# Optimization experiments

Hardware: AMD Instinct MI355X
Metric: run time of the kernel (lower is better)

## Reference

```python
import jax, jax.numpy as jnp
import numpy as np

EPS = 1e-5

def conv2d(x, w, pad):
    # x: NCHW, w: OIHW
    return jax.lax.conv_general_dilated(
        x, w, window_strides=(1, 1), padding=[(pad, pad), (pad, pad)],
        dimension_numbers=("NCHW", "OIHW", "NCHW"))

def instnorm(x, gamma=None, beta=None):
    # per-(N,C) normalization over H,W (biased variance, like torch InstanceNorm2d)
    mu = jnp.mean(x, axis=(2, 3), keepdims=True)
    var = jnp.mean((x - mu) ** 2, axis=(2, 3), keepdims=True)
    y = (x - mu) * jax.lax.rsqrt(var + EPS)
    if gamma is not None:
        y = y * gamma[None, :, None, None] + beta[None, :, None, None]
    return y

def ode_rhs(y, W, b):
    # conv -> relu -> instance norm (no affine) -> conv_transpose(same weight) -> -1 (stable)
    z = conv2d(y, W, 1) + b[None, :, None, None]
    z = jax.nn.relu(z)
    z = instnorm(z)
    # ConvTranspose2d with weight W (in,out,kh,kw here square C,C) == conv with
    # channel-swapped, spatially flipped kernel, SAME padding.
    Wt = jnp.transpose(jnp.flip(W, axis=(2, 3)), (1, 0, 2, 3))
    z = conv2d(z, Wt, 1)
    return -z

def ode_block(y, Wbank, bbank):
    # RK4 over t_grid = linspace(0,1,5): 4 steps of dt = 0.25.
    # Piecewise-constant weights: floor(t*4) clamped -> stages 1-3 of step i use
    # bank[i]; stage 4 (at t_{i+1}) uses bank[min(i+1, 3)].
    n = Wbank.shape[0]
    dt = 1.0 / n
    for i in range(n):
        j = min(i + 1, n - 1)
        k1 = ode_rhs(y, Wbank[i], bbank[i])
        k2 = ode_rhs(y + 0.5 * dt * k1, Wbank[i], bbank[i])
        k3 = ode_rhs(y + 0.5 * dt * k2, Wbank[i], bbank[i])
        k4 = ode_rhs(y + dt * k3, Wbank[j], bbank[j])
        y = y + (dt / 6.0) * (k1 + 2.0 * k2 + 2.0 * k3 + k4)
    return y

def avgpool2(x):
    N, C, H, W = x.shape
    return x.reshape(N, C, H // 2, 2, W // 2, 2).mean(axis=(3, 5))

def forward(x, stem_w, stem_b, norm1_g, norm1_b, ode1_W, ode1_b,
            conn1_w, conn1_b, norm3_g, norm3_b, ode2_W, ode2_b,
            conn2_w, conn2_b, norm4_g, norm4_b, ode3_W, ode3_b,
            head_w, head_b):
    x = conv2d(x, stem_w, 1) + stem_b[None, :, None, None]
    x = instnorm(x, norm1_g, norm1_b)
    x = jax.nn.relu(x)
    x = ode_block(x, ode1_W, ode1_b)
    x = conv2d(x, conn1_w, 0) + conn1_b[None, :, None, None]
    x = instnorm(x, norm3_g, norm3_b)
    x = jax.nn.relu(x)
    x = avgpool2(x)
    x = ode_block(x, ode2_W, ode2_b)
    x = conv2d(x, conn2_w, 0) + conn2_b[None, :, None, None]
    x = instnorm(x, norm4_g, norm4_b)
    x = jax.nn.relu(x)
    x = avgpool2(x)
    x = ode_block(x, ode3_W, ode3_b)
    x = x.mean(axis=(2, 3))  # AdaptiveAvgPool2d(1) + Flatten -> [N, 4*ch]
    return x @ head_w.T + head_b

def setup_inputs() -> dict:
    key = jax.random.key(0)
    ks = jax.random.split(key, 16)
    ch = 64
    f = jnp.float32
    d = {
        "x": jax.random.normal(ks[0], (8, 3, 96, 96), f),
        "stem_w": jax.random.normal(ks[1], (ch, 3, 3, 3), f) * 0.1,
        "stem_b": jnp.zeros((ch,), f),
        "norm1_g": jnp.ones((ch,), f),
        "norm1_b": jnp.zeros((ch,), f),
        "ode1_W": jax.random.normal(ks[2], (4, ch, ch, 3, 3), f) * 0.1,
        "ode1_b": jnp.zeros((4, ch), f),
        "conn1_w": jax.random.normal(ks[3], (2 * ch, ch, 1, 1), f) * 0.1,
        "conn1_b": jnp.zeros((2 * ch,), f),
        "norm3_g": jnp.ones((2 * ch,), f),
        "norm3_b": jnp.zeros((2 * ch,), f),
        "ode2_W": jax.random.normal(ks[4], (4, 2 * ch, 2 * ch, 3, 3), f) * 0.1,
        "ode2_b": jnp.zeros((4, 2 * ch), f),
        "conn2_w": jax.random.normal(ks[5], (4 * ch, 2 * ch, 1, 1), f) * 0.1,
        "conn2_b": jnp.zeros((4 * ch,), f),
        "norm4_g": jnp.ones((4 * ch,), f),
        "norm4_b": jnp.zeros((4 * ch,), f),
        "ode3_W": jax.random.normal(ks[6], (4, 4 * ch, 4 * ch, 3, 3), f) * 0.1,
        "ode3_b": jnp.zeros((4, 4 * ch), f),
        "head_w": jax.random.normal(ks[7], (10, 4 * ch), f) * 0.05,
        "head_b": jnp.zeros((10,), f),
    }
    return d

def reference(x, stem_w, stem_b, norm1_g, norm1_b, ode1_W, ode1_b,
              conn1_w, conn1_b, norm3_g, norm3_b, ode2_W, ode2_b,
              conn2_w, conn2_b, norm4_g, norm4_b, ode3_W, ode3_b,
              head_w, head_b):
    return forward(x, stem_w, stem_b, norm1_g, norm1_b, ode1_W, ode1_b,
                   conn1_w, conn1_b, norm3_g, norm3_b, ode2_W, ode2_b,
                   conn2_w, conn2_b, norm4_g, norm4_b, ode3_W, ode3_b,
                   head_w, head_b)
```

## Files before the change

### kernel.cpp

```cpp
#include <hip/hip_runtime.h>


typedef __attribute__((ext_vector_type(8)))  short  s16x8;
typedef __attribute__((ext_vector_type(16))) float  f32x16;

__device__ __forceinline__ unsigned short bf16_rtne(float f) {
    unsigned u = __builtin_bit_cast(unsigned, f);
    unsigned r = u + 0x7FFFu + ((u >> 16) & 1u);
    return (unsigned short)(r >> 16);
}
__device__ __forceinline__ void split2(float v, unsigned& h, unsigned& l) {
    unsigned u = __builtin_bit_cast(unsigned, v);
    h = (u + 0x7fffu + ((u >> 16) & 1u)) >> 16;
    float r = v - __builtin_bit_cast(float, h << 16);
    unsigned ur = __builtin_bit_cast(unsigned, r);
    l = (ur + 0x7fffu + ((ur >> 16) & 1u)) >> 16;
}
__device__ __forceinline__ unsigned packsplit(float v) {
    unsigned h, l; split2(v, h, l); return h | (l << 16);
}

__global__ __launch_bounds__(256) void pack_weights(
    const float* __restrict__ Wb, unsigned short* __restrict__ out, int C)
{
    const int dir = blockIdx.y;
    const int MT = C >> 5, ICC = C >> 4;
    const size_t TOT = (size_t)36 * C * C;
    size_t t = (size_t)blockIdx.x * 256 + threadIdx.x;
    if (t >= TOT) return;
    int j = t & 7;
    int l = (t >> 3) & 63;
    size_t r = t >> 9;
    int kp  = r % 9;  r /= 9;
    int mt  = r % MT; r /= MT;
    int icc = r % ICC; r /= ICC;
    int bank = (int)r;
    int oc = mt * 32 + (l & 31);
    int ic = icc * 16 + (l >> 5) * 8 + j;
    int kh = kp / 3, kw = kp % 3;
    float v;
    if (dir == 0)
        v = Wb[(((size_t)(bank * C + oc) * C + ic) * 3 + kh) * 3 + kw];
    else
        v = Wb[(((size_t)(bank * C + ic) * C + oc) * 3 + (2 - kh)) * 3 + (2 - kw)];
    unsigned short h = bf16_rtne(v);
    float hf = __builtin_bit_cast(float, (unsigned)h << 16);
    unsigned short lo = bf16_rtne(v - hf);
    size_t idx = ((((size_t)bank * ICC + icc) * MT + mt) * 9 + kp) * 1024 + l * 8 + j;
    unsigned short* base = out + (size_t)dir * 72 * C * C;
    base[idx] = h;
    base[idx + 512] = lo;
}

template<int NW, int MODE>
__global__ __launch_bounds__(NW * 64) void conv_mfma4(
    const void* __restrict__ in,
    const unsigned short* __restrict__ pA,
    const float* __restrict__ bias,
    const float* __restrict__ partI,
    float* __restrict__ partO,
    const float* __restrict__ ybase, float* __restrict__ accb,
    float* __restrict__ ydstF, unsigned* __restrict__ ydstS,
    int C, int H, int W, int tilesX, int tilesT, float inv_hw,
    int mode, float acoef, float dt6)
{
    constexpr bool CONV2 = (MODE == 2);
    constexpr int TPX = 16, TPY = 2 * NW;
    constexpr int HX = TPX + 2, HY = TPY + 2;
    constexpr int NROW = HX * HY;
    constexpr int RS = 20;
    constexpr int PL = NROW * RS;
    constexpr int BUFS = 2 * PL;
    constexpr int NTHR = NW * 64;
    constexpr int NELEM = NROW * 16;
    constexpr int NIT = (NELEM + NTHR - 1) / NTHR;
    __shared__ __align__(16) unsigned short sB[2 * BUFS];
    __shared__ float sTab[CONV2 ? 512 : 4];

    const int tid = threadIdx.x;
    const int w = tid >> 6, lane = tid & 63;
    const int n = blockIdx.x;
    const int tile = blockIdx.y;
    const int mt = blockIdx.z;
    const int tileX = tile % tilesX, tileY = tile / tilesX;
    const int px0 = tileX * TPX, py0 = tileY * TPY;
    const int ocb = mt * 32;
    const int HW = H * W;
    const int ICC = C >> 4, MT = C >> 5;
    const int col = lane & 31, half = lane >> 5;
    const int xl = col & 15, yr = col >> 4;
    const int wy0 = 2 * w;
    const int ncbase = n * C;

    float stg[NIT];
    auto stageLoad = [&](int icc) {
#pragma unroll
        for (int i = 0; i < NIT; i++) {
            int e = tid + i * NTHR;
            float v = 0.f;
            if (e < NELEM) {
                int ic = e / NROW; int r = e - ic * NROW;
                int yy = r / HX, xx = r - yy * HX;
                int gy = py0 + yy - 1, gx = px0 + xx - 1;
                if (gy >= 0 && gy < H && gx >= 0 && gx < W) {
                    int c = icc * 16 + ic;
                    size_t ad = (size_t)(ncbase + c) * HW + gy * W + gx;
                    if (MODE == 0)
                        v = ((const float*)in)[ad];
                    else
                        v = __builtin_bit_cast(float, ((const unsigned*)in)[ad]);
                }
            }
            stg[i] = v;
        }
    };
    auto stageWrite = [&](int b, int c0) {
#pragma unroll
        for (int i = 0; i < NIT; i++) {
            int e = tid + i * NTHR;
            if (e < NELEM) {
                int ic = e / NROW; int r = e - ic * NROW;
                unsigned h, l;
                if (MODE == 1) {
                    unsigned u = __builtin_bit_cast(unsigned, stg[i]);
                    h = u & 0xffffu; l = u >> 16;
                } else if (MODE == 2) {
                    int yy = r / HX, xx = r - yy * HX;
                    int gy = py0 + yy - 1, gx = px0 + xx - 1;
                    float v = 0.f;
                    if (gy >= 0 && gy < H && gx >= 0 && gx < W) {
                        unsigned u = __builtin_bit_cast(unsigned, stg[i]);
                        float vh = __builtin_bit_cast(float, u << 16);
                        float vl = __builtin_bit_cast(float, u & 0xffff0000u);
                        int c = c0 + ic;
                        v = (vh + vl - sTab[2 * c]) * sTab[2 * c + 1];
                    }
                    split2(v, h, l);
                } else {
                    split2(stg[i], h, l);
                }
                int off = b * BUFS + r * RS + ic;
                sB[off] = (unsigned short)h;
                sB[off + PL] = (unsigned short)l;
            }
        }
    };
    auto loadB = [&](int b, int kp, s16x8& oh, s16x8& ol) {
        int kh = kp / 3, kw = kp - kh * 3;
        int px = (wy0 + yr + kh) * HX + (xl + kw);
        int off = b * BUFS + px * RS + half * 8;
        oh = *(const s16x8*)&sB[off];
        ol = *(const s16x8*)&sB[off + PL];
    };

    f32x16 accA{}, accB{}, accC{};

    stageLoad(0);

    if (CONV2) {
        float* sRed = (float*)sB;
        const int g = NTHR / C;
        {
            int c0 = tid % C, sl = tid / C;
            int mtc = c0 >> 5, occ = c0 & 31;
            int t0 = (tilesT * sl) / g, t1 = (tilesT * (sl + 1)) / g;
            const float* pb = partI + ((size_t)(n * MT + mtc) * tilesT) * 64 + occ;
            float S = 0.f, Q = 0.f;
            for (int tt = t0; tt < t1; ++tt) {
                S += pb[(size_t)tt * 64];
                Q += pb[(size_t)tt * 64 + 32];
            }
            sRed[tid] = S;
            sRed[NTHR + tid] = Q;
        }
        __syncthreads();
        if (tid < C) {
            float s = 0.f, q = 0.f;
            for (int k = 0; k < g; ++k) {
                s += sRed[k * C + tid];
                q += sRed[NTHR + k * C + tid];
            }
            float m = s * inv_hw;
            sTab[2 * tid] = m;
            sTab[2 * tid + 1] = rsqrtf(fmaf(-m, m, q * inv_hw) + 1e-5f);
        }
        __syncthreads();
    }

    stageWrite(0, 0);
    __syncthreads();

    for (int icc = 0; icc < ICC; ++icc) {
        s16x8 aH[9], aL[9];
        {
            const unsigned short* ab =
                pA + ((size_t)(icc * MT + mt)) * 9216 + lane * 8;
#pragma unroll
            for (int kp = 0; kp < 9; ++kp) {
                aH[kp] = *(const s16x8*)(ab + kp * 1024);
                aL[kp] = *(const s16x8*)(ab + kp * 1024 + 512);
            }
        }
        const int b = icc & 1;
        if (icc + 1 < ICC) stageLoad(icc + 1);

        s16x8 bh, bl;
        loadB(b, 0, bh, bl);
#pragma unroll
        for (int kp = 0; kp < 9; ++kp) {
            s16x8 bhn, bln;
            if (kp < 8) loadB(b, kp + 1, bhn, bln);
            accA = __builtin_amdgcn_mfma_f32_32x32x16_bf16(aH[kp], bh, accA, 0, 0, 0);
            accB = __builtin_amdgcn_mfma_f32_32x32x16_bf16(aL[kp], bh, accB, 0, 0, 0);
            accC = __builtin_amdgcn_mfma_f32_32x32x16_bf16(aH[kp], bl, accC, 0, 0, 0);
            if (kp < 8) { bh = bhn; bl = bln; }
        }
        if (icc + 1 < ICC) {
            stageWrite(b ^ 1, (icc + 1) * 16);
            __syncthreads();
        }
    }

    const int gx = px0 + xl;
    const int gy = py0 + wy0 + yr;
    const bool valid = (gx < W);
    float* sred = (float*)sB;
#pragma unroll
    for (int r = 0; r < 16; r++) {
        int row = (r & 3) + 8 * (r >> 2) + 4 * half;
        int oc = ocb + row;
        size_t idx = (size_t)(ncbase + oc) * HW + (size_t)gy * W + gx;
        float v = accA[r] + accB[r] + accC[r];
        if (!CONV2) {
            v += bias[oc];
            v = fmaxf(v, 0.f);
            if (valid) ydstS[idx] = packsplit(v);
            float s = valid ? v : 0.f;
            float sq = s * s;
#pragma unroll
            for (int m = 1; m < 32; m <<= 1) {
                s  += __shfl_xor(s, m, 64);
                sq += __shfl_xor(sq, m, 64);
            }
            if ((lane & 31) == 0) {
                int slot = ((w * 2 + half) * 16 + r) * 2;
                sred[slot] = s;
                sred[slot + 1] = sq;
            }
        } else if (valid) {
            float k = -v;
            if (mode == 0) {
                accb[idx] = k;
                ydstS[idx] = packsplit(ybase[idx] + acoef * k);
            } else if (mode == 3) {
                ydstF[idx] = ybase[idx] + dt6 * (accb[idx] + k);
            } else {
                accb[idx] += 2.f * k;
                ydstS[idx] = packsplit(ybase[idx] + acoef * k);
            }
        }
    }
    if (!CONV2) {
        __syncthreads();
        if (tid < 32) {
            int h2 = (tid >> 2) & 1;
            int r  = (tid & 3) | ((tid >> 3) << 2);
            float s = 0.f, sq = 0.f;
#pragma unroll
            for (int wv = 0; wv < NW; wv++) {
                int slot = ((wv * 2 + h2) * 16 + r) * 2;
                s  += sred[slot];
                sq += sred[slot + 1];
            }
            float* po = partO + ((size_t)(n * MT + mt) * tilesT + tile) * 64;
            po[tid] = s;
            po[tid + 32] = sq;
        }
    }
}

__global__ __launch_bounds__(256) void conv3x3_stem(
    const float* __restrict__ in, const float* __restrict__ w,
    const float* __restrict__ bias, float* __restrict__ out,
    int H, int W, int tilesX)
{
    __shared__ float sIn[3][18][34];
    __shared__ float sW[16][3][9];
    const int tid = threadIdx.x;
    const int tx = tid & 15, ty = tid >> 4;
    const int tileX = blockIdx.x % tilesX, tileY = blockIdx.x / tilesX;
    const int x0 = tileX * 32, y0 = tileY * 16;
    const int oc0 = blockIdx.y * 16;
    const int n = blockIdx.z;
    const int HW = H * W;

    for (int idx = tid; idx < 3 * 18 * 34; idx += 256) {
        int c = idx / (18 * 34); int r = idx % (18 * 34);
        int iy = r / 34, ix = r % 34;
        int gy = y0 + iy - 1, gx = x0 + ix - 1;
        float v = 0.f;
        if (gy >= 0 && gy < H && gx >= 0 && gx < W)
            v = in[(size_t)(n * 3 + c) * HW + gy * W + gx];
        sIn[c][iy][ix] = v;
    }
    for (int idx = tid; idx < 16 * 27; idx += 256) {
        int o = idx / 27, r = idx % 27;
        sW[o][r / 9][r % 9] = w[(size_t)(oc0 + o) * 27 + r];
    }
    __syncthreads();

    float a0[16], a1[16];
#pragma unroll
    for (int o = 0; o < 16; o++) { a0[o] = 0.f; a1[o] = 0.f; }
#pragma unroll
    for (int c = 0; c < 3; c++)
#pragma unroll
        for (int kh = 0; kh < 3; kh++)
#pragma unroll
            for (int kw = 0; kw < 3; kw++) {
                float v0 = sIn[c][ty + kh][tx + kw];
                float v1 = sIn[c][ty + kh][tx + 16 + kw];
#pragma unroll
                for (int o = 0; o < 16; o++) {
                    float wv = sW[o][c][kh * 3 + kw];
                    a0[o] = fmaf(v0, wv, a0[o]);
                    a1[o] = fmaf(v1, wv, a1[o]);
                }
            }

    const int gy = y0 + ty, gx = x0 + tx;
#pragma unroll
    for (int o = 0; o < 16; o++) {
        float bb = bias[oc0 + o];
        size_t base = (size_t)(n * 64 + oc0 + o) * HW + (size_t)gy * W + gx;
        out[base] = a0[o] + bb;
        out[base + 16] = a1[o] + bb;
    }
}

__global__ __launch_bounds__(256) void stats_kernel(
    const float* __restrict__ x, float* __restrict__ mu, float* __restrict__ rstd,
    int HW, float inv_hw)
{
    int nc = blockIdx.x;
    const float* p = x + (size_t)nc * HW;
    float s = 0.f, ss = 0.f;
    for (int i = threadIdx.x; i < HW; i += 256) {
        float v = p[i];
        s += v;
        ss = fmaf(v, v, ss);
    }
    for (int off = 32; off; off >>= 1) {
        s  += __shfl_down(s, off, 64);
        ss += __shfl_down(ss, off, 64);
    }
    __shared__ float aS[4], aSS[4];
    int wid = threadIdx.x >> 6, lane = threadIdx.x & 63;
    if (lane == 0) { aS[wid] = s; aSS[wid] = ss; }
    __syncthreads();
    if (threadIdx.x == 0) {
        s  = aS[0] + aS[1] + aS[2] + aS[3];
        ss = aSS[0] + aSS[1] + aSS[2] + aSS[3];
        float m = s * inv_hw;
        float var = fmaf(-m, m, ss * inv_hw);
        mu[nc] = m;
        rstd[nc] = rsqrtf(var + 1e-5f);
    }
}

__global__ __launch_bounds__(256) void norm_affine_relu_kernel(
    const float* __restrict__ in, float* __restrict__ out,
    const float* __restrict__ mu, const float* __restrict__ rstd,
    const float* __restrict__ g, const float* __restrict__ b,
    int C, int HW, size_t total)
{
    size_t i = (size_t)blockIdx.x * 256 + threadIdx.x;
    if (i >= total) return;
    size_t nc = i / HW;
    int c = (int)(nc % C);
    float v = (in[i] - mu[nc]) * rstd[nc] * g[c] + b[c];
    out[i] = fmaxf(v, 0.f);
}

__global__ __launch_bounds__(256) void norm_pool_kernel(
    const float* __restrict__ in, float* __restrict__ out,
    const float* __restrict__ mu, const float* __restrict__ rstd,
    const float* __restrict__ g, const float* __restrict__ b,
    int C, int Ho, int Wo, size_t total)
{
    size_t i = (size_t)blockIdx.x * 256 + threadIdx.x;
    if (i >= total) return;
    int wo = (int)(i % Wo);
    int ho = (int)((i / Wo) % Ho);
    size_t nc = i / ((size_t)Wo * Ho);
    int c = (int)(nc % C);
    const int Wi = 2 * Wo;
    const float* p = in + nc * (size_t)(4 * Ho * Wo) + (size_t)(2 * ho) * Wi + 2 * wo;
    float sc  = rstd[nc] * g[c];
    float off = fmaf(-mu[nc], sc, b[c]);
    float2 t0 = *(const float2*)p;
    float2 t1 = *(const float2*)(p + Wi);
    float s = fmaxf(fmaf(t0.x, sc, off), 0.f) + fmaxf(fmaf(t0.y, sc, off), 0.f)
            + fmaxf(fmaf(t1.x, sc, off), 0.f) + fmaxf(fmaf(t1.y, sc, off), 0.f);
    out[i] = 0.25f * s;
}

#define C1OCT 8
__global__ __launch_bounds__(256) void conv1x1_kernel(
    const float* __restrict__ in, const float* __restrict__ w,
    const float* __restrict__ bias, float* __restrict__ out,
    int Cin, int Cout, int HW)
{
    const int HW4 = HW >> 2;
    int p = blockIdx.x * 256 + threadIdx.x;
    if (p >= HW4) return;
    const int oc0 = blockIdx.y * C1OCT;
    const int n = blockIdx.z;
    const float4* ip = (const float4*)(in + (size_t)n * Cin * HW) + p;
    float acc[C1OCT][4];
#pragma unroll
    for (int o = 0; o < C1OCT; o++)
        acc[o][0] = acc[o][1] = acc[o][2] = acc[o][3] = 0.f;
#pragma unroll 4
    for (int ic = 0; ic < Cin; ic++) {
        float4 v = ip[(size_t)ic * HW4];
#pragma unroll
        for (int o = 0; o < C1OCT; o++) {
            float wv = w[(size_t)(oc0 + o) * Cin + ic];
            acc[o][0] = fmaf(v.x, wv, acc[o][0]);
            acc[o][1] = fmaf(v.y, wv, acc[o][1]);
            acc[o][2] = fmaf(v.z, wv, acc[o][2]);
            acc[o][3] = fmaf(v.w, wv, acc[o][3]);
        }
    }
    float4* op = (float4*)(out + ((size_t)n * Cout + oc0) * HW) + p;
#pragma unroll
    for (int o = 0; o < C1OCT; o++) {
        float bb = bias[oc0 + o];
        float4 r;
        r.x = acc[o][0] + bb; r.y = acc[o][1] + bb;
        r.z = acc[o][2] + bb; r.w = acc[o][3] + bb;
        op[(size_t)o * HW4] = r;
    }
}

__global__ __launch_bounds__(128) void head_kernel(
    const float* __restrict__ m, const float* __restrict__ hw,
    const float* __restrict__ hb, float* __restrict__ out, int C)
{
    int t = threadIdx.x;
    if (t < 80) {
        int n = t / 10, k = t % 10;
        float acc = hb[k];
        for (int c = 0; c < C; c++)
            acc = fmaf(m[n * C + c], hw[k * C + c], acc);
        out[t] = acc;
    }
}

struct OdeCfg { int C, H, tilesX, tilesT; };
static const OdeCfg CFG[3] = {
    {64, 96, 6, 72},
    {128, 48, 3, 18},
    {256, 24, 2, 6},
};

static void launch_c1(int st, int inMode, const void* in, const unsigned short* pA,
                      const float* bias, float* part, unsigned* z, hipStream_t s)
{
    const OdeCfg& c = CFG[st];
    dim3 g(8, c.tilesT, c.C / 32);
    float ih = 1.f / (c.H * c.H);
    if (inMode == 0)
        conv_mfma4<4, 0><<<g, 256, 0, s>>>(in, pA, bias,
            nullptr, part, nullptr, nullptr, nullptr, z,
            c.C, c.H, c.H, c.tilesX, c.tilesT, ih, 0, 0.f, 0.f);
    else
        conv_mfma4<4, 1><<<g, 256, 0, s>>>(in, pA, bias,
            nullptr, part, nullptr, nullptr, nullptr, z,
            c.C, c.H, c.H, c.tilesX, c.tilesT, ih, 0, 0.f, 0.f);
}

static void launch_c2(int st, const unsigned* z, const unsigned short* pA,
                      const float* part,
                      const float* ybase, float* accb,
                      float* ydstF, unsigned* ydstS,
                      int mode, float acoef, hipStream_t s)
{
    const OdeCfg& c = CFG[st];
    dim3 g(8, c.tilesT, c.C / 32);
    float ih = 1.f / (c.H * c.H);
    const float dt6 = 0.25f / 6.f;
    conv_mfma4<4, 2><<<g, 256, 0, s>>>(z, pA, nullptr,
        part, nullptr, ybase, accb, ydstF, ydstS,
        c.C, c.H, c.H, c.tilesX, c.tilesT, ih, mode, acoef, dt6);
}

static void ode_block_mfma(int st, float* y, unsigned* t, unsigned* z, float* a,
                           float* part, unsigned short* pack,
                           const float* bbank, hipStream_t s)
{
    const OdeCfg& c = CFG[st];
    const int C = c.C;
    const size_t BANKW = (size_t)18 * C * C;
    const size_t DIRW  = (size_t)72 * C * C;
    const float dt = 0.25f;
    for (int i = 0; i < 4; i++) {
        int j = (i + 1 > 3) ? 3 : i + 1;
        const unsigned short* p1  = pack + i * BANKW;
        const unsigned short* p1t = pack + DIRW + i * BANKW;
        const unsigned short* p4  = pack + j * BANKW;
        const unsigned short* p4t = pack + DIRW + j * BANKW;
        const float* b1 = bbank + (size_t)i * C;
        const float* b4 = bbank + (size_t)j * C;

        launch_c1(st, 0, y, p1, b1, part, z, s);
        launch_c2(st, z, p1t, part, y, a, nullptr, t, 0, 0.5f * dt, s);
        launch_c1(st, 1, t, p1, b1, part, z, s);
        launch_c2(st, z, p1t, part, y, a, nullptr, t, 1, 0.5f * dt, s);
        launch_c1(st, 1, t, p1, b1, part, z, s);
        launch_c2(st, z, p1t, part, y, a, nullptr, t, 1, dt, s);
        launch_c1(st, 1, t, p4, b4, part, z, s);
        launch_c2(st, z, p4t, part, y, a, y, t, 3, 0.f, s);
    }
}

extern "C" void kernel_launch(void* const* d_in, const int* in_sizes, int n_in,
                              void* d_out, int out_size, void* d_ws, size_t ws_size,
                              hipStream_t stream)
{
    const float* x       = (const float*)d_in[0];
    const float* stem_w  = (const float*)d_in[1];
    const float* stem_b  = (const float*)d_in[2];
    const float* norm1_g = (const float*)d_in[3];
    const float* norm1_b = (const float*)d_in[4];
    const float* ode1_W  = (const float*)d_in[5];
    const float* ode1_b  = (const float*)d_in[6];
    const float* conn1_w = (const float*)d_in[7];
    const float* conn1_b = (const float*)d_in[8];
    const float* norm3_g = (const float*)d_in[9];
    const float* norm3_b = (const float*)d_in[10];
    const float* ode2_W  = (const float*)d_in[11];
    const float* ode2_b  = (const float*)d_in[12];
    const float* conn2_w = (const float*)d_in[13];
    const float* conn2_b = (const float*)d_in[14];
    const float* norm4_g = (const float*)d_in[15];
    const float* norm4_b = (const float*)d_in[16];
    const float* ode3_W  = (const float*)d_in[17];
    const float* ode3_b  = (const float*)d_in[18];
    const float* head_w  = (const float*)d_in[19];
    const float* head_b  = (const float*)d_in[20];
    float* out = (float*)d_out;

    float* ws = (float*)d_ws;
    const size_t BUF = 4718592;
    float*    y  = ws;
    unsigned* t  = (unsigned*)(ws + BUF);
    unsigned* z  = (unsigned*)(ws + 2 * BUF);
    float*    a  = ws + 3 * BUF;
    float*    mu = ws + 4 * BUF;
    float*    rs = mu + 2048;
    float*    part = ws + 4 * BUF + 4096;
    unsigned short* pack = (unsigned short*)(ws + 4 * BUF + 4096 + 73728);
    float* tf = (float*)t;

    {
        int H = 96;
        dim3 grid(3 * 6, 4, 8);
        conv3x3_stem<<<grid, 256, 0, stream>>>(x, stem_w, stem_b, (float*)z,
                                               H, H, 3);
        stats_kernel<<<8 * 64, 256, 0, stream>>>((float*)z, mu, rs, H * H, 1.f / (H * H));
        size_t total = (size_t)8 * 64 * H * H;
        norm_affine_relu_kernel<<<(total + 255) / 256, 256, 0, stream>>>(
            (float*)z, y, mu, rs, norm1_g, norm1_b, 64, H * H, total);
    }

    {
        size_t TOT = (size_t)36 * 64 * 64;
        pack_weights<<<dim3((TOT + 255) / 256, 2), 256, 0, stream>>>(ode1_W, pack, 64);
        ode_block_mfma(0, y, t, z, a, part, pack, ode1_b, stream);
    }

    {
        int H = 96, HW = H * H, Cin = 64, Cout = 128;
        dim3 grid((HW / 4 + 255) / 256, Cout / C1OCT, 8);
        conv1x1_kernel<<<grid, 256, 0, stream>>>(y, conn1_w, conn1_b, tf, Cin, Cout, HW);
        stats_kernel<<<8 * Cout, 256, 0, stream>>>(tf, mu, rs, HW, 1.f / HW);
        size_t ptotal = (size_t)8 * Cout * 48 * 48;
        norm_pool_kernel<<<(ptotal + 255) / 256, 256, 0, stream>>>(
            tf, y, mu, rs, norm3_g, norm3_b, Cout, 48, 48, ptotal);
    }

    {
        size_t TOT = (size_t)36 * 128 * 128;
        pack_weights<<<dim3((TOT + 255) / 256, 2), 256, 0, stream>>>(ode2_W, pack, 128);
        ode_block_mfma(1, y, t, z, a, part, pack, ode2_b, stream);
    }

    {
        int H = 48, HW = H * H, Cin = 128, Cout = 256;
        dim3 grid((HW / 4 + 255) / 256, Cout / C1OCT, 8);
        conv1x1_kernel<<<grid, 256, 0, stream>>>(y, conn2_w, conn2_b, tf, Cin, Cout, HW);
        stats_kernel<<<8 * Cout, 256, 0, stream>>>(tf, mu, rs, HW, 1.f / HW);
        size_t ptotal = (size_t)8 * Cout * 24 * 24;
        norm_pool_kernel<<<(ptotal + 255) / 256, 256, 0, stream>>>(
            tf, y, mu, rs, norm4_g, norm4_b, Cout, 24, 24, ptotal);
    }

    {
        size_t TOT = (size_t)36 * 256 * 256;
        pack_weights<<<dim3((TOT + 255) / 256, 2), 256, 0, stream>>>(ode3_W, pack, 256);
        ode_block_mfma(2, y, t, z, a, part, pack, ode3_b, stream);
    }

    {
        int H = 24, HW = H * H, C = 256;
        stats_kernel<<<8 * C, 256, 0, stream>>>(y, mu, rs, HW, 1.f / HW);
        head_kernel<<<1, 128, 0, stream>>>(mu, head_w, head_b, out, C);
    }
}
```

Before: 5.332 ms.

## Compute two 32-channel output tiles per block to reuse staged input tiles

Each conv block now computes 64 output channels (two MFMA M-tiles) instead of 32, halving the grid's z dimension. The input halo tile staged in LDS, and its bf16 hi/lo split, is reused across both output tiles, which halves input staging and global reads per output. Weight fragments are now loaded inside the kp loop instead of being preloaded per icc. This doubles accumulator registers, may lower occupancy, and cuts the block count, which hurts most for the smaller stages.

```diff
diff --git a/kernel.cpp b/kernel.cpp
--- a/kernel.cpp
+++ b/kernel.cpp
@@ -81,10 +81,11 @@
     const int w = tid >> 6, lane = tid & 63;
     const int n = blockIdx.x;
     const int tile = blockIdx.y;
-    const int mt = blockIdx.z;
+    const int mtz = blockIdx.z;
+    const int mt0 = 2 * mtz;
     const int tileX = tile % tilesX, tileY = tile / tilesX;
     const int px0 = tileX * TPX, py0 = tileY * TPY;
-    const int ocb = mt * 32;
+    const int ocb0 = mt0 * 32;
     const int HW = H * W;
     const int ICC = C >> 4, MT = C >> 5;
     const int col = lane & 31, half = lane >> 5;
@@ -153,7 +154,8 @@
         ol = *(const s16x8*)&sB[off + PL];
     };
 
-    f32x16 accA{}, accB{}, accC{};
+    f32x16 accA0{}, accB0{}, accC0{};
+    f32x16 accA1{}, accB1{}, accC1{};
 
     stageLoad(0);
 
@@ -191,18 +193,12 @@
     __syncthreads();
 
     for (int icc = 0; icc < ICC; ++icc) {
-        s16x8 aH[9], aL[9];
-        {
-            const unsigned short* ab =
-                pA + ((size_t)(icc * MT + mt)) * 9216 + lane * 8;
-#pragma unroll
-            for (int kp = 0; kp < 9; ++kp) {
-                aH[kp] = *(const s16x8*)(ab + kp * 1024);
-                aL[kp] = *(const s16x8*)(ab + kp * 1024 + 512);
-            }
-        }
         const int b = icc & 1;
         if (icc + 1 < ICC) stageLoad(icc + 1);
+
+        const unsigned short* ab0 =
+            pA + ((size_t)(icc * MT + mt0)) * 9216 + lane * 8;
+        const unsigned short* ab1 = ab0 + 9216;
 
         s16x8 bh, bl;
         loadB(b, 0, bh, bl);
@@ -210,9 +206,16 @@
         for (int kp = 0; kp < 9; ++kp) {
             s16x8 bhn, bln;
             if (kp < 8) loadB(b, kp + 1, bhn, bln);
-            accA = __builtin_amdgcn_mfma_f32_32x32x16_bf16(aH[kp], bh, accA, 0, 0, 0);
-            accB = __builtin_amdgcn_mfma_f32_32x32x16_bf16(aL[kp], bh, accB, 0, 0, 0);
-            accC = __builtin_amdgcn_mfma_f32_32x32x16_bf16(aH[kp], bl, accC, 0, 0, 0);
+            s16x8 aH0 = *(const s16x8*)(ab0 + kp * 1024);
+            s16x8 aL0 = *(const s16x8*)(ab0 + kp * 1024 + 512);
+            accA0 = __builtin_amdgcn_mfma_f32_32x32x16_bf16(aH0, bh, accA0, 0, 0, 0);
+            accB0 = __builtin_amdgcn_mfma_f32_32x32x16_bf16(aL0, bh, accB0, 0, 0, 0);
+            accC0 = __builtin_amdgcn_mfma_f32_32x32x16_bf16(aH0, bl, accC0, 0, 0, 0);
+            s16x8 aH1 = *(const s16x8*)(ab1 + kp * 1024);
+            s16x8 aL1 = *(const s16x8*)(ab1 + kp * 1024 + 512);
+            accA1 = __builtin_amdgcn_mfma_f32_32x32x16_bf16(aH1, bh, accA1, 0, 0, 0);
+            accB1 = __builtin_amdgcn_mfma_f32_32x32x16_bf16(aL1, bh, accB1, 0, 0, 0);
+            accC1 = __builtin_amdgcn_mfma_f32_32x32x16_bf16(aH1, bl, accC1, 0, 0, 0);
             if (kp < 8) { bh = bhn; bl = bln; }
         }
         if (icc + 1 < ICC) {
@@ -225,56 +228,65 @@
     const int gy = py0 + wy0 + yr;
     const bool valid = (gx < W);
     float* sred = (float*)sB;
-#pragma unroll
-    for (int r = 0; r < 16; r++) {
-        int row = (r & 3) + 8 * (r >> 2) + 4 * half;
-        int oc = ocb + row;
-        size_t idx = (size_t)(ncbase + oc) * HW + (size_t)gy * W + gx;
-        float v = accA[r] + accB[r] + accC[r];
-        if (!CONV2) {
-            v += bias[oc];
-            v = fmaxf(v, 0.f);
-            if (valid) ydstS[idx] = packsplit(v);
-            float s = valid ? v : 0.f;
-            float sq = s * s;
-#pragma unroll
-            for (int m = 1; m < 32; m <<= 1) {
-                s  += __shfl_xor(s, m, 64);
-                sq += __shfl_xor(sq, m, 64);
+
+    auto epi = [&](const f32x16& eA, const f32x16& eB, const f32x16& eC,
+                   int ocb, int mtw) {
+#pragma unroll
+        for (int r = 0; r < 16; r++) {
+            int row = (r & 3) + 8 * (r >> 2) + 4 * half;
+            int oc = ocb + row;
+            size_t idx = (size_t)(ncbase + oc) * HW + (size_t)gy * W + gx;
+            float v = eA[r] + eB[r] + eC[r];
+            if (!CONV2) {
+                v += bias[oc];
+                v = fmaxf(v, 0.f);
+                if (valid) ydstS[idx] = packsplit(v);
+                float s = valid ? v : 0.f;
+                float sq = s * s;
+#pragma unroll
+                for (int m = 1; m < 32; m <<= 1) {
+                    s  += __shfl_xor(s, m, 64);
+                    sq += __shfl_xor(sq, m, 64);
+                }
+                if ((lane & 31) == 0) {
+                    int slot = (((mtw * NW + w) * 2 + half) * 16 + r) * 2;
+                    sred[slot] = s;
+                    sred[slot + 1] = sq;
+                }
+            } else if (valid) {
+                float k = -v;
+                if (mode == 0) {
+                    accb[idx] = k;
+                    ydstS[idx] = packsplit(ybase[idx] + acoef * k);
+                } else if (mode == 3) {
+                    ydstF[idx] = ybase[idx] + dt6 * (accb[idx] + k);
+                } else {
+                    accb[idx] += 2.f * k;
+                    ydstS[idx] = packsplit(ybase[idx] + acoef * k);
+                }
             }
-            if ((lane & 31) == 0) {
-                int slot = ((w * 2 + half) * 16 + r) * 2;
-                sred[slot] = s;
-                sred[slot + 1] = sq;
-            }
-        } else if (valid) {
-            float k = -v;
-            if (mode == 0) {
-                accb[idx] = k;
-                ydstS[idx] = packsplit(ybase[idx] + acoef * k);
-            } else if (mode == 3) {
-                ydstF[idx] = ybase[idx] + dt6 * (accb[idx] + k);
-            } else {
-                accb[idx] += 2.f * k;
-                ydstS[idx] = packsplit(ybase[idx] + acoef * k);
-            }
-        }
-    }
+        }
+    };
+    epi(accA0, accB0, accC0, ocb0, 0);
+    epi(accA1, accB1, accC1, ocb0 + 32, 1);
+
     if (!CONV2) {
         __syncthreads();
-        if (tid < 32) {
-            int h2 = (tid >> 2) & 1;
-            int r  = (tid & 3) | ((tid >> 3) << 2);
+        if (tid < 64) {
+            int mtw = tid >> 5, t5 = tid & 31;
+            int h2 = (t5 >> 2) & 1;
+            int r  = (t5 & 3) | ((t5 >> 3) << 2);
             float s = 0.f, sq = 0.f;
 #pragma unroll
             for (int wv = 0; wv < NW; wv++) {
-                int slot = ((wv * 2 + h2) * 16 + r) * 2;
+                int slot = (((mtw * NW + wv) * 2 + h2) * 16 + r) * 2;
                 s  += sred[slot];
                 sq += sred[slot + 1];
             }
+            int mt = mt0 + mtw;
             float* po = partO + ((size_t)(n * MT + mt) * tilesT + tile) * 64;
-            po[tid] = s;
-            po[tid + 32] = sq;
+            po[t5] = s;
+            po[t5 + 32] = sq;
         }
     }
 }
@@ -469,7 +481,7 @@
                       const float* bias, float* part, unsigned* z, hipStream_t s)
 {
     const OdeCfg& c = CFG[st];
-    dim3 g(8, c.tilesT, c.C / 32);
+    dim3 g(8, c.tilesT, c.C / 64);
     float ih = 1.f / (c.H * c.H);
     if (inMode == 0)
         conv_mfma4<4, 0><<<g, 256, 0, s>>>(in, pA, bias,
@@ -488,7 +500,7 @@
                       int mode, float acoef, hipStream_t s)
 {
     const OdeCfg& c = CFG[st];
-    dim3 g(8, c.tilesT, c.C / 32);
+    dim3 g(8, c.tilesT, c.C / 64);
     float ih = 1.f / (c.H * c.H);
     const float dt6 = 0.25f / 6.f;
     conv_mfma4<4, 2><<<g, 256, 0, s>>>(z, pA, nullptr,
```

Measured after the change: 7.506 ms. 40.8% more time.
